# Optimization experiments

Hardware: AMD Instinct MI355X
Metric: run time of the kernel (lower is better)

Reference implementation:

```python
import jax, jax.numpy as jnp
import numpy as np

N = 50000        # num nodes
E = 800000       # num edges (no self loops by construction)
D = 128          # in_features == out_features
NE = 4           # num_envs
EPS = 1e-8
STDV = 1.0 / np.sqrt(D)


def setup_inputs() -> dict:
    key = jax.random.key(0)
    k = jax.random.split(key, 6)
    x = jax.random.normal(k[0], (N, D), jnp.float32)
    row = jax.random.randint(k[1], (E,), 0, N, dtype=jnp.int32)
    off = jax.random.randint(k[2], (E,), 1, N, dtype=jnp.int32)
    col = (row + off) % N  # guarantees no self loops (matches remove_self_loops)
    adj = jnp.stack([row, col])
    env_weights = jax.random.uniform(k[3], (N, NE), jnp.float32)
    weights = jax.random.uniform(k[4], (NE, D, D), jnp.float32, -STDV, STDV)
    a = jax.random.normal(k[5], (NE, 2 * D, 1), jnp.float32) * np.sqrt(2.0 / (2 * D + 1)) * 1.414
    return {"x": x, "adj": adj, "env_weights": env_weights, "weights": weights, "a": a}


def reference(x, adj, env_weights, weights, a):
    n = x.shape[0]
    f = weights.shape[-1]
    loops = jnp.arange(n, dtype=adj.dtype)
    src = jnp.concatenate([adj[0], loops])  # add_self_loops
    dst = jnp.concatenate([adj[1], loops])
    # per-env projected features: [NE, N, F]
    h = jnp.einsum('nd,edf->enf', x, weights)
    # attention logits: cat(h[src], h[dst]) @ a  ==  h[src]@a1 + h[dst]@a2
    a1 = a[:, :f, 0]   # [NE, F]
    a2 = a[:, f:, 0]   # [NE, F]
    s_src = jnp.einsum('enf,ef->en', h, a1)
    s_dst = jnp.einsum('enf,ef->en', h, a2)
    logits = jax.nn.leaky_relu(s_src[:, src] + s_dst[:, dst], 0.01)  # [NE, Etot]
    # global per-env max subtraction (as in the torch code: max over all edges)
    e = jnp.exp(logits - jnp.max(logits, axis=1, keepdims=True))
    def agg(ek, hk):
        # specialspmm: out[src] += ek * hk[dst]; denom via ones vector
        denom = jax.ops.segment_sum(ek, src, num_segments=n) + EPS          # [N]
        num = jax.ops.segment_sum(ek[:, None] * hk[dst], src, num_segments=n)  # [N, F]
        return num / denom[:, None]
    out_env = jax.vmap(agg)(e, h)  # [NE, N, F]
    out = jnp.einsum('ne,enf->nf', env_weights, out_env)
    return out + x  # residual
```

## Files before the change

### kernel.cpp

```cpp
#include <hip/hip_runtime.h>

#define N_NODES 50000
#define N_EDGES 800000
#define D_FEAT  128
#define NE_ENV  4
#define EPS_F   1e-8f
#define M_CONST 4.0f
#define NB_BUCKET 391
#define BINA_EPT 16
#define NBH 200
#define EH  4000

typedef __attribute__((ext_vector_type(8))) short bf16x8;
typedef __attribute__((ext_vector_type(4))) float floatx4;
typedef __attribute__((ext_vector_type(2))) float f32x2;

static __device__ __forceinline__ unsigned short f2bf(float v) {
    union { float f; unsigned int u; } c; c.f = v;
    unsigned int u = c.u;
    u += 0x7fffu + ((u >> 16) & 1u);
    return (unsigned short)(u >> 16);
}

static __device__ __forceinline__ f32x2 bf2f(unsigned int v) {
    f32x2 r;
    r.x = __uint_as_float(v << 16);
    r.y = __uint_as_float(v & 0xffff0000u);
    return r;
}

static __device__ __forceinline__ float lrelu_exp(float z) {
    float lk = z > 0.f ? z : 0.01f * z;
    return __expf(lk - M_CONST);
}

static __device__ __forceinline__ void pk_add(f32x2& acc, f32x2 w) {
    asm("v_pk_add_f32 %0, %1, %0" : "+v"(acc) : "v"(w));
}
static __device__ __forceinline__ void pk_fma_bl(f32x2& acc, f32x2 w, f32x2 x) {
    asm("v_pk_fma_f32 %0, %1, %2, %0 op_sel:[0,0,0] op_sel_hi:[0,1,1]" : "+v"(acc) : "v"(w), "v"(x));
}
static __device__ __forceinline__ void pk_fma_bh(f32x2& acc, f32x2 w, f32x2 x) {
    asm("v_pk_fma_f32 %0, %1, %2, %0 op_sel:[1,0,0] op_sel_hi:[1,1,1]" : "+v"(acc) : "v"(w), "v"(x));
}

static __device__ __forceinline__ void edge_acc(unsigned int xv, float4 w,
        f32x2& den01, f32x2& den23, f32x2* axy) {
    f32x2 x = bf2f(xv);
    f32x2 wxy; wxy.x = w.x; wxy.y = w.y;
    f32x2 wzw; wzw.x = w.z; wzw.y = w.w;
    pk_add(den01, wxy);
    pk_add(den23, wzw);
    pk_fma_bl(axy[0], wxy, x);
    pk_fma_bh(axy[1], wxy, x);
    pk_fma_bl(axy[2], wzw, x);
    pk_fma_bh(axy[3], wzw, x);
}

__global__ __launch_bounds__(256) void k_setup(const float* __restrict__ weights, const float* __restrict__ a,
        float* __restrict__ b, unsigned short* __restrict__ wsw,
        const int* __restrict__ row, int* __restrict__ bcnt) {
    int blk = blockIdx.x;
    if (blk < 128) {
        int wave = threadIdx.x >> 6, lane = threadIdx.x & 63;
        int t = blk * 4 + wave;
        int e = t >> 7, d = t & 127;
        float2 w2 = ((const float2*)(weights + e * 16384 + d * 128))[lane];
        float2 a1 = ((const float2*)(a + e * 256))[lane];
        float2 a2 = ((const float2*)(a + e * 256 + 128))[lane];
        float p1 = w2.x * a1.x + w2.y * a1.y;
        float p2 = w2.x * a2.x + w2.y * a2.y;
#pragma unroll
        for (int off = 32; off > 0; off >>= 1) {
            p1 += __shfl_xor(p1, off, 64);
            p2 += __shfl_xor(p2, off, 64);
        }
        if (lane == 0) {
            b[e * 128 + d] = p1;
            b[512 + e * 128 + d] = p2;
        }
    } else if (blk < 384) {
        int idx = (blk - 128) * 256 + threadIdx.x;
        int j = idx & 7;
        int l = (idx >> 3) & 63;
        int t = (idx >> 9) & 7;
        int s = idx >> 12;
        int k = s * 32 + (l >> 4) * 8 + j;
        int f = t * 16 + (l & 15);
        int e = k >> 7, d = k & 127;
        wsw[idx] = f2bf(weights[e * 16384 + d * 128 + f]);
    } else {
        __shared__ int h[NB_BUCKET];
        int t = threadIdx.x;
        for (int i = t; i < NB_BUCKET; i += 256) h[i] = 0;
        __syncthreads();
        int e0 = (blk - 384) * EH;
        for (int j = t; j < EH; j += 256) {
            int k = e0 + j;
            if (k < N_EDGES) atomicAdd(&h[row[k] >> 7], 1);
        }
        __syncthreads();
        for (int i = t; i < NB_BUCKET; i += 256) {
            int c = h[i];
            if (c) atomicAdd(&bcnt[i], c);
        }
    }
}

__global__ __launch_bounds__(256) void k_s(const float* __restrict__ x, const float* __restrict__ b,
        float* __restrict__ s_src, float* __restrict__ s_dst, unsigned short* __restrict__ xbf) {
    int wave = threadIdx.x >> 6, lane = threadIdx.x & 63;
    int gw = blockIdx.x * 4 + wave;
    if (gw >= 3125) return;
    int quad = lane >> 4, lm = lane & 15;
    int base = gw * 16;

    floatx4 acc = (floatx4){0.f, 0.f, 0.f, 0.f};
    const float* xrow = x + (size_t)(base + lm) * 128 + quad * 8;
    unsigned short* xbrow = xbf + (size_t)(base + lm) * 128 + quad * 8;

#pragma unroll
    for (int s = 0; s < 4; ++s) {
        float4 lo = *(const float4*)(xrow + s * 32);
        float4 hi = *(const float4*)(xrow + s * 32 + 4);
        bf16x8 af;
        af[0] = (short)f2bf(lo.x); af[1] = (short)f2bf(lo.y);
        af[2] = (short)f2bf(lo.z); af[3] = (short)f2bf(lo.w);
        af[4] = (short)f2bf(hi.x); af[5] = (short)f2bf(hi.y);
        af[6] = (short)f2bf(hi.z); af[7] = (short)f2bf(hi.w);
        *(bf16x8*)(xbrow + s * 32) = af;

        bf16x8 bfv = (bf16x8){0, 0, 0, 0, 0, 0, 0, 0};
        if (lm < 8) {
            const float* bp = b + lm * 128 + s * 32 + quad * 8;
            float4 b0 = *(const float4*)bp;
            float4 b1 = *(const float4*)(bp + 4);
            bfv[0] = (short)f2bf(b0.x); bfv[1] = (short)f2bf(b0.y);
            bfv[2] = (short)f2bf(b0.z); bfv[3] = (short)f2bf(b0.w);
            bfv[4] = (short)f2bf(b1.x); bfv[5] = (short)f2bf(b1.y);
            bfv[6] = (short)f2bf(b1.z); bfv[7] = (short)f2bf(b1.w);
        }
        acc = __builtin_amdgcn_mfma_f32_16x16x32_bf16(af, bfv, acc, 0, 0, 0);
    }
    if (lm < 8) {
        float* dstp = (lm < 4) ? (s_src + (size_t)(base + quad * 4) * 4 + lm)
                               : (s_dst + (size_t)(base + quad * 4) * 4 + (lm - 4));
#pragma unroll
        for (int r = 0; r < 4; ++r) dstp[r * 4] = acc[r];
    }
}

__global__ void k_bscan(const int* __restrict__ bcnt, int* __restrict__ bbase,
                        int* __restrict__ bcur, int* __restrict__ offsets) {
    __shared__ int sm[512];
    int t = threadIdx.x;
    int v = (t < NB_BUCKET) ? bcnt[t] : 0;
    sm[t] = v;
    __syncthreads();
    for (int s2 = 1; s2 < 512; s2 <<= 1) {
        int add = (t >= s2) ? sm[t - s2] : 0;
        __syncthreads();
        sm[t] += add;
        __syncthreads();
    }
    int excl = sm[t] - v;
    if (t < NB_BUCKET) { bbase[t] = excl; bcur[t] = excl; }
    if (t == NB_BUCKET) bbase[t] = excl;
    if (t == 0) offsets[N_NODES] = N_EDGES;
}

__global__ __launch_bounds__(256) void k_binA(const int* __restrict__ row, const int* __restrict__ col,
        int* __restrict__ bcur, unsigned int* __restrict__ binned) {
    __shared__ int cnt[NB_BUCKET];
    __shared__ int base[NB_BUCKET];
    int t = threadIdx.x;
    for (int b = t; b < NB_BUCKET; b += 256) cnt[b] = 0;
    __syncthreads();
    unsigned int pk[BINA_EPT];
    int ebase = blockIdx.x * (256 * BINA_EPT) + t;
#pragma unroll
    for (int j = 0; j < BINA_EPT; ++j) {
        int k = ebase + j * 256;
        pk[j] = 0xffffffffu;
        if (k < N_EDGES) {
            unsigned int s = (unsigned int)row[k];
            unsigned int d = (unsigned int)col[k];
            pk[j] = (s << 16) | d;
            atomicAdd(&cnt[s >> 7], 1);
        }
    }
    __syncthreads();
    for (int b = t; b < NB_BUCKET; b += 256) {
        int c = cnt[b];
        base[b] = c ? atomicAdd(&bcur[b], c) : 0;
        cnt[b] = 0;
    }
    __syncthreads();
#pragma unroll
    for (int j = 0; j < BINA_EPT; ++j) {
        if (pk[j] != 0xffffffffu) {
            int b = pk[j] >> 23;
            int off = atomicAdd(&cnt[b], 1);
            binned[base[b] + off] = pk[j];
        }
    }
}

__global__ __launch_bounds__(256) void k_binB(const unsigned int* __restrict__ binned,
        const int* __restrict__ bbase,
        const float* __restrict__ s_src, const float* __restrict__ s_dst,
        int* __restrict__ offsets, int* __restrict__ sorted_dst, float4* __restrict__ w_sorted) {
    __shared__ int hist[128];
    __shared__ int cur[128];
    int b = blockIdx.x;
    int nb = b << 7;
    int nc = min(128, N_NODES - nb);
    int t = threadIdx.x;
    if (t < 128) hist[t] = 0;
    __syncthreads();
    int ebeg = bbase[b];
    int eend = bbase[b + 1];
    for (int i = ebeg + t; i < eend; i += 256)
        atomicAdd(&hist[(binned[i] >> 16) & 127], 1);
    __syncthreads();
    int v = (t < 128) ? hist[t] : 0;
    for (int s2 = 1; s2 < 128; s2 <<= 1) {
        int add = (t >= s2 && t < 128) ? hist[t - s2] : 0;
        __syncthreads();
        if (t < 128) hist[t] += add;
        __syncthreads();
    }
    if (t < 128) {
        int pos = ebeg + hist[t] - v;
        cur[t] = pos;
        if (t < nc) offsets[nb + t] = pos;
    }
    __syncthreads();
    for (int i = ebeg + t; i < eend; i += 256) {
        unsigned int pk = binned[i];
        int s = (int)(pk >> 16), d = (int)(pk & 0xffffu);
        float4 a4 = *(const float4*)(s_src + s * 4);
        float4 b4 = *(const float4*)(s_dst + d * 4);
        float4 w;
        w.x = lrelu_exp(a4.x + b4.x);
        w.y = lrelu_exp(a4.y + b4.y);
        w.z = lrelu_exp(a4.z + b4.z);
        w.w = lrelu_exp(a4.w + b4.w);
        int pos = atomicAdd(&cur[s & 127], 1);
        sorted_dst[pos] = d;
        w_sorted[pos] = w;
    }
}

__global__ __launch_bounds__(512) void k_agg_gemm(const unsigned int* __restrict__ xb,
        const float* __restrict__ s_src, const float* __restrict__ s_dst,
        const int* __restrict__ offsets, const int* __restrict__ sorted_dst,
        const float4* __restrict__ w_sorted, const float* __restrict__ env_w,
        const unsigned short* __restrict__ Wsw,
        const float* __restrict__ x, float* __restrict__ out) {
    __shared__ __align__(16) unsigned int Gsm[32 * 256];
    int wave = threadIdx.x >> 6, lane = threadIdx.x & 63;
    int nb = blockIdx.x * 32;

#pragma unroll 1
    for (int j = 0; j < 4; ++j) {
        int r = wave * 4 + j;
        int n = nb + r;
        int swz = (r & 7) << 2;
        if (n >= N_NODES) {
#pragma unroll
            for (int e = 0; e < 4; ++e) Gsm[(r * 256 + e * 64 + lane) ^ swz] = 0;
            continue;
        }

        f32x2 den01, den23;
        f32x2 axy[4];
        {
            float4 sa = *(const float4*)(s_src + n * 4);
            float4 sb = *(const float4*)(s_dst + n * 4);
            float ws0 = lrelu_exp(sa.x + sb.x), ws1 = lrelu_exp(sa.y + sb.y);
            float ws2 = lrelu_exp(sa.z + sb.z), ws3 = lrelu_exp(sa.w + sb.w);
            f32x2 xv = bf2f(xb[((unsigned)n << 6) + lane]);
            den01.x = ws0; den01.y = ws1;
            den23.x = ws2; den23.y = ws3;
            axy[0].x = ws0 * xv.x; axy[0].y = ws0 * xv.y;
            axy[1].x = ws1 * xv.x; axy[1].y = ws1 * xv.y;
            axy[2].x = ws2 * xv.x; axy[2].y = ws2 * xv.y;
            axy[3].x = ws3 * xv.x; axy[3].y = ws3 * xv.y;
        }

        int beg = __builtin_amdgcn_readfirstlane(offsets[n]);
        int end = __builtin_amdgcn_readfirstlane(offsets[n + 1]);
        int i = beg;
        for (; i + 7 < end; i += 8) {
            int d[8]; float4 w[8]; unsigned int v[8];
#pragma unroll
            for (int q = 0; q < 8; ++q) d[q] = sorted_dst[i + q];
#pragma unroll
            for (int q = 0; q < 8; ++q) v[q] = xb[((unsigned)d[q] << 6) + lane];
#pragma unroll
            for (int q = 0; q < 8; ++q) w[q] = w_sorted[i + q];
#pragma unroll
            for (int q = 0; q < 8; ++q) edge_acc(v[q], w[q], den01, den23, axy);
        }
        for (; i + 3 < end; i += 4) {
            int d[4]; float4 w[4]; unsigned int v[4];
#pragma unroll
            for (int q = 0; q < 4; ++q) d[q] = sorted_dst[i + q];
#pragma unroll
            for (int q = 0; q < 4; ++q) v[q] = xb[((unsigned)d[q] << 6) + lane];
#pragma unroll
            for (int q = 0; q < 4; ++q) w[q] = w_sorted[i + q];
#pragma unroll
            for (int q = 0; q < 4; ++q) edge_acc(v[q], w[q], den01, den23, axy);
        }
        for (; i < end; ++i) {
            int d0 = sorted_dst[i];
            edge_acc(xb[((unsigned)d0 << 6) + lane], w_sorted[i], den01, den23, axy);
        }

        float4 ewt = *(const float4*)(env_w + n * 4);
        float ewv[4] = { ewt.x, ewt.y, ewt.z, ewt.w };
        float dens[4] = { den01.x, den01.y, den23.x, den23.y };
#pragma unroll
        for (int e = 0; e < 4; ++e) {
            float sc = ewv[e] / (dens[e] + EPS_F);
            unsigned int lo = f2bf(sc * axy[e].x);
            unsigned int hi = f2bf(sc * axy[e].y);
            Gsm[(r * 256 + e * 64 + lane) ^ swz] = (hi << 16) | lo;
        }
    }
    __syncthreads();

    int quad = lane >> 4, lm = lane & 15;
    int cb = wave;
    bf16x8 Bf[16];
#pragma unroll
    for (int s = 0; s < 16; ++s)
        Bf[s] = *(const bf16x8*)(Wsw + (((s * 8 + cb) * 64 + lane) * 8));
    int rswz = (lm & 7) << 2;
#pragma unroll
    for (int rt = 0; rt < 2; ++rt) {
        floatx4 acc = (floatx4){0.f, 0.f, 0.f, 0.f};
#pragma unroll
        for (int s = 0; s < 16; ++s) {
            int idx = (((rt * 16 + lm) * 256 + s * 16 + quad * 4) ^ rswz);
            bf16x8 af = *(const bf16x8*)(&Gsm[idx]);
            acc = __builtin_amdgcn_mfma_f32_16x16x32_bf16(af, Bf[s], acc, 0, 0, 0);
        }
        int row_base = nb + rt * 16 + quad * 4;
        int c = cb * 16 + lm;
#pragma unroll
        for (int r = 0; r < 4; ++r) {
            int rowi = row_base + r;
            if (rowi < N_NODES) out[rowi * 128 + c] = acc[r] + x[rowi * 128 + c];
        }
    }
}

extern "C" void kernel_launch(void* const* d_in, const int* in_sizes, int n_in,
                              void* d_out, int out_size, void* d_ws, size_t ws_size,
                              hipStream_t stream) {
    const float* x       = (const float*)d_in[0];
    const int*   adj     = (const int*)d_in[1];
    const int*   row     = adj;
    const int*   col     = adj + N_EDGES;
    const float* env_w   = (const float*)d_in[2];
    const float* weights = (const float*)d_in[3];
    const float* a       = (const float*)d_in[4];
    float* out = (float*)d_out;

    char* ws = (char*)d_ws;
    size_t off = 0;
    auto alloc = [&](size_t bytes) -> char* {
        char* p = ws + off;
        off += (bytes + 255) & ~(size_t)255;
        return p;
    };
    float* b          = (float*)alloc(1024 * 4);
    float* s_src      = (float*)alloc((size_t)N_NODES * 4 * 4);
    float* s_dst      = (float*)alloc((size_t)N_NODES * 4 * 4);
    int*   offsets    = (int*)alloc((size_t)(N_NODES + 1) * 4);
    int*   bcnt       = (int*)alloc(512 * 4);
    int*   bbase      = (int*)alloc(512 * 4);
    int*   bcur       = (int*)alloc(512 * 4);
    unsigned int* binned = (unsigned int*)alloc((size_t)N_EDGES * 4);
    int*   sorted_dst = (int*)alloc((size_t)N_EDGES * 4);
    float4* w_sorted  = (float4*)alloc((size_t)N_EDGES * 16);
    unsigned short* wsw = (unsigned short*)alloc(65536 * 2);
    unsigned short* xbf = (unsigned short*)alloc((size_t)N_NODES * 128 * 2);

    hipMemsetAsync(bcnt, 0, 512 * 4, stream);
    k_setup<<<384 + NBH, 256, 0, stream>>>(weights, a, b, wsw, row, bcnt);
    k_s<<<782, 256, 0, stream>>>(x, b, s_src, s_dst, xbf);
    k_bscan<<<1, 512, 0, stream>>>(bcnt, bbase, bcur, offsets);
    k_binA<<<196, 256, 0, stream>>>(row, col, bcur, binned);
    k_binB<<<NB_BUCKET, 256, 0, stream>>>(binned, bbase, s_src, s_dst, offsets, sorted_dst, w_sorted);
    k_agg_gemm<<<1563, 512, 0, stream>>>((const unsigned int*)xbf, s_src, s_dst, offsets,
                                         sorted_dst, w_sorted, env_w, wsw, x, out);
}
```

Measured before the change: 208.1 us.

## Shrink agg-GEMM tile to 16 nodes per 256-thread block

Halves the per-block node tile from 32 to 16 rows and the block size from 512 to 256 threads, doubling the grid. Each wave now computes two 16-column output tiles for one 16-row tile, streaming the weight fragments from global memory in the loop rather than preloading 16 fragments into registers. Bounds checks are removed because 50000 divides evenly by 16. The intent is to cut register pressure and LDS per block so more blocks stay resident to hide gather latency, at the cost of reloading the weights more often across blocks.

```diff
diff --git a/kernel.cpp b/kernel.cpp
--- a/kernel.cpp
+++ b/kernel.cpp
@@ -252,26 +252,20 @@
     }
 }
 
-__global__ __launch_bounds__(512) void k_agg_gemm(const unsigned int* __restrict__ xb,
+__global__ __launch_bounds__(256) void k_agg_gemm(const unsigned int* __restrict__ xb,
         const float* __restrict__ s_src, const float* __restrict__ s_dst,
         const int* __restrict__ offsets, const int* __restrict__ sorted_dst,
         const float4* __restrict__ w_sorted, const float* __restrict__ env_w,
         const unsigned short* __restrict__ Wsw,
         const float* __restrict__ x, float* __restrict__ out) {
-    __shared__ __align__(16) unsigned int Gsm[32 * 256];
+    __shared__ __align__(16) unsigned int Gsm[16 * 256];
     int wave = threadIdx.x >> 6, lane = threadIdx.x & 63;
-    int nb = blockIdx.x * 32;
+    int nb = blockIdx.x * 16;
 
 #pragma unroll 1
     for (int j = 0; j < 4; ++j) {
         int r = wave * 4 + j;
         int n = nb + r;
-        int swz = (r & 7) << 2;
-        if (n >= N_NODES) {
-#pragma unroll
-            for (int e = 0; e < 4; ++e) Gsm[(r * 256 + e * 64 + lane) ^ swz] = 0;
-            continue;
-        }
 
         f32x2 den01, den23;
         f32x2 axy[4];
@@ -322,6 +316,7 @@
         float4 ewt = *(const float4*)(env_w + n * 4);
         float ewv[4] = { ewt.x, ewt.y, ewt.z, ewt.w };
         float dens[4] = { den01.x, den01.y, den23.x, den23.y };
+        int swz = (r & 7) << 2;
 #pragma unroll
         for (int e = 0; e < 4; ++e) {
             float sc = ewv[e] / (dens[e] + EPS_F);
@@ -333,28 +328,27 @@
     __syncthreads();
 
     int quad = lane >> 4, lm = lane & 15;
-    int cb = wave;
-    bf16x8 Bf[16];
-#pragma unroll
-    for (int s = 0; s < 16; ++s)
-        Bf[s] = *(const bf16x8*)(Wsw + (((s * 8 + cb) * 64 + lane) * 8));
+    int t0 = wave * 2;
+    floatx4 acc0 = (floatx4){0.f, 0.f, 0.f, 0.f};
+    floatx4 acc1 = (floatx4){0.f, 0.f, 0.f, 0.f};
     int rswz = (lm & 7) << 2;
 #pragma unroll
-    for (int rt = 0; rt < 2; ++rt) {
-        floatx4 acc = (floatx4){0.f, 0.f, 0.f, 0.f};
-#pragma unroll
-        for (int s = 0; s < 16; ++s) {
-            int idx = (((rt * 16 + lm) * 256 + s * 16 + quad * 4) ^ rswz);
-            bf16x8 af = *(const bf16x8*)(&Gsm[idx]);
-            acc = __builtin_amdgcn_mfma_f32_16x16x32_bf16(af, Bf[s], acc, 0, 0, 0);
-        }
-        int row_base = nb + rt * 16 + quad * 4;
-        int c = cb * 16 + lm;
-#pragma unroll
-        for (int r = 0; r < 4; ++r) {
-            int rowi = row_base + r;
-            if (rowi < N_NODES) out[rowi * 128 + c] = acc[r] + x[rowi * 128 + c];
-        }
+    for (int s = 0; s < 16; ++s) {
+        int idx = (lm * 256 + s * 16 + quad * 4) ^ rswz;
+        bf16x8 af = *(const bf16x8*)(&Gsm[idx]);
+        bf16x8 b0 = *(const bf16x8*)(Wsw + (((s * 8 + t0) * 64 + lane) * 8));
+        bf16x8 b1 = *(const bf16x8*)(Wsw + (((s * 8 + t0 + 1) * 64 + lane) * 8));
+        acc0 = __builtin_amdgcn_mfma_f32_16x16x32_bf16(af, b0, acc0, 0, 0, 0);
+        acc1 = __builtin_amdgcn_mfma_f32_16x16x32_bf16(af, b1, acc1, 0, 0, 0);
+    }
+    int row_base = nb + quad * 4;
+#pragma unroll
+    for (int r = 0; r < 4; ++r) {
+        int rowi = row_base + r;
+        int c0 = t0 * 16 + lm;
+        int c1 = c0 + 16;
+        out[rowi * 128 + c0] = acc0[r] + x[rowi * 128 + c0];
+        out[rowi * 128 + c1] = acc1[r] + x[rowi * 128 + c1];
     }
 }
 
@@ -396,6 +390,6 @@
     k_bscan<<<1, 512, 0, stream>>>(bcnt, bbase, bcur, offsets);
     k_binA<<<196, 256, 0, stream>>>(row, col, bcur, binned);
     k_binB<<<NB_BUCKET, 256, 0, stream>>>(binned, bbase, s_src, s_dst, offsets, sorted_dst, w_sorted);
-    k_agg_gemm<<<1563, 512, 0, stream>>>((const unsigned int*)xbf, s_src, s_dst, offsets,
+    k_agg_gemm<<<3125, 256, 0, stream>>>((const unsigned int*)xbf, s_src, s_dst, offsets,
                                          sorted_dst, w_sorted, env_w, wsw, x, out);
 }
```

Measured after the change: 189.0 us. -9.2%, faster.
